# Optimization experiments

Hardware: AMD Instinct MI355X
Metric: run time of the kernel (lower is better)

## Reference

```python
import jax, jax.numpy as jnp
import numpy as np

DIM = 768
NUM_BLOCKS = 4
BLOCK = DIM // NUM_BLOCKS
SCALE = 0.02


def setup_inputs() -> dict:
    key = jax.random.key(0)
    ks = jax.random.split(key, 7)
    x = jax.random.normal(ks[0], (8, 64, 64, DIM), dtype=jnp.float32)
    w1 = SCALE * jax.random.normal(ks[1], (2, NUM_BLOCKS, BLOCK, BLOCK), dtype=jnp.float32)
    b1 = SCALE * jax.random.normal(ks[2], (2, NUM_BLOCKS, BLOCK), dtype=jnp.float32)
    w2 = SCALE * jax.random.normal(ks[3], (2, NUM_BLOCKS, BLOCK, BLOCK), dtype=jnp.float32)
    b2 = SCALE * jax.random.normal(ks[4], (2, NUM_BLOCKS, BLOCK), dtype=jnp.float32)
    # nn.Linear(dim, dim) weight/bias (kaiming-uniform-ish init; exact init irrelevant for correctness)
    lim = 1.0 / np.sqrt(DIM)
    bias_w = jax.random.uniform(ks[5], (DIM, DIM), minval=-lim, maxval=lim, dtype=jnp.float32)
    bias_b = jax.random.uniform(ks[6], (DIM,), minval=-lim, maxval=lim, dtype=jnp.float32)
    return {"x": x, "w1": w1, "b1": b1, "w2": w2, "b2": b2, "bias_w": bias_w, "bias_b": bias_b}


def _block_mul(t, w):
    # t: (..., nb, bs), w: (nb, bs, bs) -> (..., nb, bs)
    return jnp.einsum('...bd,bdk->...bk', t, w)


def reference(x, w1, b1, w2, b2, bias_w, bias_b):
    B, H, W, C = x.shape
    nb = w1.shape[1]
    bs = C // nb
    bias = x @ bias_w.T + bias_b  # nn.Linear on original x
    xb = x.reshape(B, H, W, nb, bs)
    xf = jnp.fft.rfftn(xb, axes=(1, 2), norm='ortho')  # (B, H, W//2+1, nb, bs) complex
    xr, xi = xf.real, xf.imag
    # layer 1: complex block matmul + bias + relu (relu applied per real/imag part as in source)
    r1 = jax.nn.relu(_block_mul(xr, w1[0]) - _block_mul(xi, w1[1]) + b1[0])
    i1 = jax.nn.relu(_block_mul(xr, w1[1]) + _block_mul(xi, w1[0]) + b1[1])
    # layer 2: NOTE the original torch code reassigns x_real first and then uses the NEW
    # x_real when computing x_imag — we faithfully reproduce that.
    r2 = _block_mul(r1, w2[0]) - _block_mul(i1, w2[1]) + b2[0]
    i2 = _block_mul(r2, w2[1]) + _block_mul(i1, w2[0]) + b2[1]
    xc = jax.lax.complex(r2, i2)
    out = jnp.fft.irfftn(xc, s=(H, W), axes=(1, 2), norm='ortho')
    out = out.reshape(B, H, W, C)
    return out + bias
```

## Files before the change

### kernel.cpp

```cpp
#include <hip/hip_runtime.h>

#define DIM 768
#define NBLK 4
#define BS 192
#define BATCH 8
#define HH 64
#define WW 64
#define KH 33
#define NPTS (BATCH*HH*KH)
#define TWOPI_OVER_64 0.0981747704246810387f
#define LROW 200
#define WSZ (NBLK*BS*BS)

typedef __attribute__((ext_vector_type(8))) short short8;
typedef __attribute__((ext_vector_type(4))) short short4v;
typedef __attribute__((ext_vector_type(4))) float floatx4;
typedef __attribute__((ext_vector_type(4))) unsigned int uint4v;

static __device__ __forceinline__ short f2bs(float f) {
  union { float f; unsigned int i; } v; v.f = f;
  unsigned int x = v.i;
  return (short)((x + 0x7fffu + ((x >> 16) & 1u)) >> 16);
}
static __device__ __forceinline__ float bs2f(short s) {
  union { unsigned int i; float f; } v; v.i = ((unsigned int)(unsigned short)s) << 16; return v.f;
}

#define GLD16(gp, lp) \
  __builtin_amdgcn_global_load_lds( \
      (const __attribute__((address_space(1))) unsigned int*)(gp), \
      (__attribute__((address_space(3))) unsigned int*)(lp), 16, 0, 0)

__global__ __launch_bounds__(256) void k_convx(
    const float* __restrict__ X, short* __restrict__ Xb)
{
  const int i = blockIdx.x * 256 + threadIdx.x;
  const float4* X4 = (const float4*)X;
  #pragma unroll
  for (int it = 0; it < 12; ++it) {
    const int idx = i + it * (2048 * 256);
    const float4 v = X4[idx];
    short4v p = { f2bs(v.x), f2bs(v.y), f2bs(v.z), f2bs(v.w) };
    *(short4v*)&Xb[(size_t)idx * 4] = p;
  }
}

__global__ __launch_bounds__(256) void k_convw(
    const float* __restrict__ W, short* __restrict__ Wb)
{
  const int idx = blockIdx.x * 256 + threadIdx.x;
  const float4 v = ((const float4*)W)[idx];
  short4v p = { f2bs(v.x), f2bs(v.y), f2bs(v.z), f2bs(v.w) };
  *(short4v*)&Wb[(size_t)idx * 4] = p;
}

__global__ __launch_bounds__(256) void k_bias_gemm3(
    const short* __restrict__ Xb, const short* __restrict__ Wb,
    const float* __restrict__ bb, short* __restrict__ Bias)
{
  __shared__ short As[128 * 32];
  __shared__ short Bs[128 * 32];
  const int t = threadIdx.x;
  const int wave = t >> 6, lane = t & 63;
  const int qm = lane & 15, quad = lane >> 4;
  const int wr = (wave >> 1) * 64;
  const int wc = (wave & 1) * 64;
  const int m0 = blockIdx.x * 128, n0 = blockIdx.y * 128;

  floatx4 acc[4][4];
  const floatx4 zero = {0.f, 0.f, 0.f, 0.f};
  #pragma unroll
  for (int ms = 0; ms < 4; ++ms)
    #pragma unroll
    for (int ns = 0; ns < 4; ++ns) acc[ms][ns] = zero;

  const int r0 = t >> 2,        kq0 = (t & 3) * 8;
  const int r1 = (t + 256) >> 2;
  const short* gA0 = &Xb[(size_t)(m0 + r0) * DIM + kq0];
  const short* gA1 = &Xb[(size_t)(m0 + r1) * DIM + kq0];
  const short* gB0 = &Wb[(size_t)(n0 + r0) * DIM + kq0];
  const short* gB1 = &Wb[(size_t)(n0 + r1) * DIM + kq0];
  short* lA0 = &As[wave * 512];
  short* lA1 = &As[wave * 512 + 2048];
  short* lB0 = &Bs[wave * 512];
  short* lB1 = &Bs[wave * 512 + 2048];

  #pragma unroll 1
  for (int k0 = 0; k0 < DIM; k0 += 32) {
    __syncthreads();
    GLD16(gA0 + k0, lA0);
    GLD16(gA1 + k0, lA1);
    GLD16(gB0 + k0, lB0);
    GLD16(gB1 + k0, lB1);
    __syncthreads();

    short8 af[4], bf[4];
    #pragma unroll
    for (int ms = 0; ms < 4; ++ms)
      af[ms] = *(const short8*)&As[(wr + ms*16 + qm) * 32 + quad * 8];
    #pragma unroll
    for (int ns = 0; ns < 4; ++ns)
      bf[ns] = *(const short8*)&Bs[(wc + ns*16 + qm) * 32 + quad * 8];
    #pragma unroll
    for (int ms = 0; ms < 4; ++ms)
      #pragma unroll
      for (int ns = 0; ns < 4; ++ns)
        acc[ms][ns] = __builtin_amdgcn_mfma_f32_16x16x32_bf16(af[ms], bf[ns], acc[ms][ns], 0, 0, 0);
  }

  #pragma unroll
  for (int ns = 0; ns < 4; ++ns) {
    const int col = n0 + wc + ns*16 + qm;
    const float bias = bb[col];
    #pragma unroll
    for (int ms = 0; ms < 4; ++ms)
      #pragma unroll
      for (int r = 0; r < 4; ++r) {
        const int row = m0 + wr + ms*16 + quad*4 + r;
        Bias[(size_t)row * DIM + col] = f2bs(acc[ms][ns][r] + bias);
      }
  }
}

__global__ __launch_bounds__(256) void k_rfft_w_mfma(
    const short* __restrict__ Xb,
    short* __restrict__ Sr, short* __restrict__ Si)
{
  __shared__ short Lx[96 * 72];
  const int t = threadIdx.x;
  const int wave = t >> 6, lane = t & 63;
  const int qm = lane & 15, quad = lane >> 4;
  const int bh = blockIdx.x;
  const int c0 = blockIdx.y * 96;
  const size_t xbase = (size_t)bh * (WW*DIM);
  const size_t obase = (size_t)bh * (KH*DIM);

  const int hd = t & 31;
  const int c4b = t >> 5;
  short4v ra[3], rb[3];
  #pragma unroll
  for (int it = 0; it < 3; ++it) {
    const int c4 = c4b + it * 8;
    const size_t g0 = xbase + (size_t)(2*hd) * DIM + c0 + c4 * 4;
    ra[it] = *(const short4v*)&Xb[g0];
    rb[it] = *(const short4v*)&Xb[g0 + DIM];
  }

  short8 Trh[2], Trl[2], Tih[2], Til[2];
  const int krow = wave * 16 + qm;
  #pragma unroll
  for (int kk = 0; kk < 2; ++kk) {
    #pragma unroll
    for (int j = 0; j < 8; ++j) {
      const int w = quad * 8 + j + kk * 32;
      const int ph = (krow * w) & 63;
      float s, c;
      sincosf((float)ph * TWOPI_OVER_64, &s, &c);
      const float tr = c, ti = -s;
      const short trh = f2bs(tr);
      const short tih = f2bs(ti);
      Trh[kk][j] = trh;  Trl[kk][j] = f2bs(tr - bs2f(trh));
      Tih[kk][j] = tih;  Til[kk][j] = f2bs(ti - bs2f(tih));
    }
  }

  #pragma unroll
  for (int it = 0; it < 3; ++it) {
    const int c4 = c4b + it * 8;
    #pragma unroll
    for (int e = 0; e < 4; ++e) {
      const int d = (c4*4 + e) * 36 + hd;
      ((unsigned*)Lx)[d] = (unsigned)(unsigned short)ra[it][e] |
                           ((unsigned)(unsigned short)rb[it][e] << 16);
    }
  }
  __syncthreads();

  if (wave < 3) {
    const floatx4 zero = {0.f, 0.f, 0.f, 0.f};
    #pragma unroll 1
    for (int ct = 0; ct < 6; ++ct) {
      floatx4 Cr = zero, Ci = zero;
      #pragma unroll
      for (int kk = 0; kk < 2; ++kk) {
        const int a = (ct*16 + qm) * 72 + kk*32 + quad*8;
        const short8 xv = *(const short8*)&Lx[a];
        Cr = __builtin_amdgcn_mfma_f32_16x16x32_bf16(Trh[kk], xv, Cr, 0,0,0);
        Cr = __builtin_amdgcn_mfma_f32_16x16x32_bf16(Trl[kk], xv, Cr, 0,0,0);
        Ci = __builtin_amdgcn_mfma_f32_16x16x32_bf16(Tih[kk], xv, Ci, 0,0,0);
        Ci = __builtin_amdgcn_mfma_f32_16x16x32_bf16(Til[kk], xv, Ci, 0,0,0);
      }
      #pragma unroll
      for (int r = 0; r < 4; ++r) {
        const int ko = wave*16 + quad*4 + r;
        if (ko < KH) {
          const size_t o = obase + (size_t)ko * DIM + c0 + ct*16 + qm;
          Sr[o] = f2bs(Cr[r]);
          Si[o] = f2bs(Ci[r]);
        }
      }
    }
  }
}

__global__ __launch_bounds__(256) void k_prep_w(
    const float* __restrict__ w1, const float* __restrict__ w2,
    short* __restrict__ Wout)
{
  const int arr = blockIdx.y;
  const int i = blockIdx.x * 256 + threadIdx.x;
  const int nb = i / (BS*BS);
  const int rem = i % (BS*BS);
  const int n = rem / BS;
  const int d = rem % BS;
  const float* src = (arr < 2) ? w1 : w2;
  const int j = arr & 1;
  const float s = (arr == 3) ? -1.f : 1.f;
  const float v = s * src[((size_t)(j*NBLK + nb) * BS + d) * BS + n];
  Wout[(size_t)arr * WSZ + i] = f2bs(v);
}

__global__ __launch_bounds__(256) void k_prep_w2(
    const float* __restrict__ w2, const float* __restrict__ b2,
    short* __restrict__ Wout, float* __restrict__ b2x)
{
  const int i = blockIdx.x * 256 + threadIdx.x;
  const int n = i % BS;
  const int d = (i / BS) % BS;
  const int nb = i / (BS*BS);
  const float* R = w2 + (size_t)nb * BS * BS;
  const float* I = w2 + ((size_t)NBLK + nb) * BS * BS;
  const float* br = b2 + nb * BS;
  float ri = 0.f, ii = 0.f, bx = 0.f;
  #pragma unroll 4
  for (int m = 0; m < BS; ++m) {
    const float win = I[m*BS + n];
    ri += R[d*BS + m] * win;
    ii += I[d*BS + m] * win;
    bx += br[m] * win;
  }
  const size_t o = ((size_t)nb * BS + n) * BS + d;
  Wout[(size_t)4 * WSZ + o] = f2bs(ri);
  Wout[(size_t)5 * WSZ + o] = f2bs(R[d*BS + n] - ii);
  if (d == 0) b2x[nb * BS + n] = b2[(NBLK + nb) * BS + n] + bx;
}

__global__ __launch_bounds__(256) void k_fmix(
    short* __restrict__ Sr, short* __restrict__ Si,
    const short* __restrict__ WT,
    const float* __restrict__ b1, const float* __restrict__ b2,
    const float* __restrict__ b2x)
{
  __shared__ short U[2 * 192 * 72];
  short* Ldr = U;
  short* Ldi = U + 192 * 72;
  short* Amr = U;
  short* Ami = U + 64 * LROW;

  const int t = threadIdx.x;
  const int wave = t >> 6, lane = t & 63;
  const int qm = lane & 15, quad = lane >> 4;
  const int bk = blockIdx.x;
  const int b = bk / KH, k = bk % KH;
  const int nb = blockIdx.y;
  const int c0 = nb * BS;
  const size_t hstride = (size_t)KH * DIM;
  const size_t base = ((size_t)b * HH * KH + k) * DIM;

  const int hd = t & 31;
  const int c8b = t >> 5;
  short8 ra[3], rb[3], ia[3], ib[3];
  #pragma unroll
  for (int it = 0; it < 3; ++it) {
    const int c8 = c8b + it * 8;
    const size_t g0 = base + (size_t)(2*hd) * hstride + c0 + c8 * 8;
    ra[it] = *(const short8*)&Sr[g0];
    rb[it] = *(const short8*)&Sr[g0 + hstride];
    ia[it] = *(const short8*)&Si[g0];
    ib[it] = *(const short8*)&Si[g0 + hstride];
  }

  const short* W1R  = WT;
  const short* W1I  = WT + 1 * (size_t)WSZ;
  const short* W2R  = WT + 2 * (size_t)WSZ;
  const short* W2IN = WT + 3 * (size_t)WSZ;
  const short* W2RI = WT + 4 * (size_t)WSZ;
  const short* W2X  = WT + 5 * (size_t)WSZ;
  int nl[3];
  size_t wb[3];
  #pragma unroll
  for (int nt = 0; nt < 3; ++nt) {
    nl[nt] = wave * 48 + nt * 16 + qm;
    wb[nt] = (size_t)(c0 + nl[nt]) * BS + quad * 8;
  }
  short8 w1r[3], w1i[3];
  #pragma unroll
  for (int nt = 0; nt < 3; ++nt) {
    w1r[nt] = *(const short8*)&W1R[wb[nt]];
    w1i[nt] = *(const short8*)&W1I[wb[nt]];
  }

  short8 Ch[2], Cl[2], Sh[2], Sl[2], SNh[2], SNl[2];
  const int hp = wave * 16 + qm;
  #pragma unroll
  for (int kk = 0; kk < 2; ++kk)
    #pragma unroll
    for (int j = 0; j < 8; ++j) {
      const int h = quad*8 + j + kk*32;
      const int ph = (hp * h) & 63;
      float s, c;
      sincosf((float)ph * TWOPI_OVER_64, &s, &c);
      const short ch = f2bs(c), sh = f2bs(s);
      Ch[kk][j] = ch;  Cl[kk][j] = f2bs(c - bs2f(ch));
      Sh[kk][j] = sh;  Sl[kk][j] = f2bs(s - bs2f(sh));
      SNh[kk][j] = (short)(sh ^ (short)0x8000);
      SNl[kk][j] = (short)(Sl[kk][j] ^ (short)0x8000);
    }

  #pragma unroll
  for (int it = 0; it < 3; ++it) {
    const int c8 = c8b + it * 8;
    #pragma unroll
    for (int e = 0; e < 8; ++e) {
      const int d = (c8*8 + e) * 36 + hd;
      ((unsigned*)Ldr)[d] = (unsigned)(unsigned short)ra[it][e] |
                            ((unsigned)(unsigned short)rb[it][e] << 16);
      ((unsigned*)Ldi)[d] = (unsigned)(unsigned short)ia[it][e] |
                            ((unsigned)(unsigned short)ib[it][e] << 16);
    }
  }
  __syncthreads();

  const floatx4 zero = {0.f, 0.f, 0.f, 0.f};
  floatx4 Fr[12], Fi[12];
  #pragma unroll
  for (int ct = 0; ct < 12; ++ct) { Fr[ct] = zero; Fi[ct] = zero; }
  #pragma unroll
  for (int ct = 0; ct < 12; ++ct)
    #pragma unroll
    for (int kk = 0; kk < 2; ++kk) {
      const int a = (ct*16 + qm) * 72 + kk*32 + quad*8;
      const short8 sr = *(const short8*)&Ldr[a];
      const short8 si = *(const short8*)&Ldi[a];
      Fr[ct] = __builtin_amdgcn_mfma_f32_16x16x32_bf16(Ch[kk],  sr, Fr[ct], 0,0,0);
      Fr[ct] = __builtin_amdgcn_mfma_f32_16x16x32_bf16(Cl[kk],  sr, Fr[ct], 0,0,0);
      Fr[ct] = __builtin_amdgcn_mfma_f32_16x16x32_bf16(Sh[kk],  si, Fr[ct], 0,0,0);
      Fr[ct] = __builtin_amdgcn_mfma_f32_16x16x32_bf16(Sl[kk],  si, Fr[ct], 0,0,0);
      Fi[ct] = __builtin_amdgcn_mfma_f32_16x16x32_bf16(SNh[kk], sr, Fi[ct], 0,0,0);
      Fi[ct] = __builtin_amdgcn_mfma_f32_16x16x32_bf16(SNl[kk], sr, Fi[ct], 0,0,0);
      Fi[ct] = __builtin_amdgcn_mfma_f32_16x16x32_bf16(Ch[kk],  si, Fi[ct], 0,0,0);
      Fi[ct] = __builtin_amdgcn_mfma_f32_16x16x32_bf16(Cl[kk],  si, Fi[ct], 0,0,0);
    }
  __syncthreads();

  #pragma unroll
  for (int ct = 0; ct < 12; ++ct)
    #pragma unroll
    for (int r = 0; r < 4; ++r) {
      const int row = wave*16 + quad*4 + r;
      const int c = ct*16 + qm;
      Amr[row * LROW + c] = f2bs(Fr[ct][r] * 0.015625f);
      Ami[row * LROW + c] = f2bs(Fi[ct][r] * 0.015625f);
    }
  __syncthreads();

  floatx4 aR[4][3], aI[4][3];
  #pragma unroll
  for (int ms = 0; ms < 4; ++ms)
    #pragma unroll
    for (int nt = 0; nt < 3; ++nt) { aR[ms][nt] = zero; aI[ms][nt] = zero; }

  #pragma unroll 1
  for (int k0 = 0; k0 < BS; k0 += 32) {
    short8 xr[4], xi[4];
    #pragma unroll
    for (int ms = 0; ms < 4; ++ms) {
      const int a = (ms*16 + qm) * LROW + k0 + quad * 8;
      xr[ms] = *(const short8*)&Amr[a];
      xi[ms] = *(const short8*)&Ami[a];
    }
    short8 cwr[3], cwi[3];
    #pragma unroll
    for (int nt = 0; nt < 3; ++nt) { cwr[nt] = w1r[nt]; cwi[nt] = w1i[nt]; }
    const int kn = k0 + 32;
    if (kn < BS) {
      #pragma unroll
      for (int nt = 0; nt < 3; ++nt) {
        w1r[nt] = *(const short8*)&W1R[wb[nt] + kn];
        w1i[nt] = *(const short8*)&W1I[wb[nt] + kn];
      }
    }
    #pragma unroll
    for (int nt = 0; nt < 3; ++nt) {
      short8 bin;
      *(uint4v*)&bin = *(const uint4v*)&cwi[nt] ^ 0x80008000u;
      #pragma unroll
      for (int ms = 0; ms < 4; ++ms) {
        aR[ms][nt] = __builtin_amdgcn_mfma_f32_16x16x32_bf16(xr[ms], cwr[nt], aR[ms][nt], 0,0,0);
        aR[ms][nt] = __builtin_amdgcn_mfma_f32_16x16x32_bf16(xi[ms], bin,     aR[ms][nt], 0,0,0);
        aI[ms][nt] = __builtin_amdgcn_mfma_f32_16x16x32_bf16(xr[ms], cwi[nt], aI[ms][nt], 0,0,0);
        aI[ms][nt] = __builtin_amdgcn_mfma_f32_16x16x32_bf16(xi[ms], cwr[nt], aI[ms][nt], 0,0,0);
      }
    }
  }
  __syncthreads();
  #pragma unroll
  for (int nt = 0; nt < 3; ++nt) {
    const float b1r = b1[nb * BS + nl[nt]];
    const float b1i = b1[(NBLK + nb) * BS + nl[nt]];
    #pragma unroll
    for (int ms = 0; ms < 4; ++ms)
      #pragma unroll
      for (int r = 0; r < 4; ++r) {
        const int row = ms*16 + quad*4 + r;
        Amr[row * LROW + nl[nt]] = f2bs(fmaxf(aR[ms][nt][r] + b1r, 0.f));
        Ami[row * LROW + nl[nt]] = f2bs(fmaxf(aI[ms][nt][r] + b1i, 0.f));
      }
  }
  __syncthreads();

  floatx4 c2r[4][3], c2i[4][3];
  #pragma unroll
  for (int ms = 0; ms < 4; ++ms)
    #pragma unroll
    for (int nt = 0; nt < 3; ++nt) { c2r[ms][nt] = zero; c2i[ms][nt] = zero; }

  #pragma unroll 1
  for (int k0 = 0; k0 < BS; k0 += 32) {
    short8 r1[4], i1[4];
    #pragma unroll
    for (int ms = 0; ms < 4; ++ms) {
      const int a = (ms*16 + qm) * LROW + k0 + quad * 8;
      r1[ms] = *(const short8*)&Amr[a];
      i1[ms] = *(const short8*)&Ami[a];
    }
    short8 w_r[3], w_in[3], w_ri[3], w_x[3];
    #pragma unroll
    for (int nt = 0; nt < 3; ++nt) {
      w_r [nt] = *(const short8*)&W2R [wb[nt] + k0];
      w_in[nt] = *(const short8*)&W2IN[wb[nt] + k0];
      w_ri[nt] = *(const short8*)&W2RI[wb[nt] + k0];
      w_x [nt] = *(const short8*)&W2X [wb[nt] + k0];
    }
    #pragma unroll
    for (int nt = 0; nt < 3; ++nt) {
      #pragma unroll
      for (int ms = 0; ms < 4; ++ms) {
        c2r[ms][nt] = __builtin_amdgcn_mfma_f32_16x16x32_bf16(r1[ms], w_r [nt], c2r[ms][nt], 0,0,0);
        c2r[ms][nt] = __builtin_amdgcn_mfma_f32_16x16x32_bf16(i1[ms], w_in[nt], c2r[ms][nt], 0,0,0);
        c2i[ms][nt] = __builtin_amdgcn_mfma_f32_16x16x32_bf16(r1[ms], w_ri[nt], c2i[ms][nt], 0,0,0);
        c2i[ms][nt] = __builtin_amdgcn_mfma_f32_16x16x32_bf16(i1[ms], w_x [nt], c2i[ms][nt], 0,0,0);
      }
    }
  }
  __syncthreads();

  #pragma unroll
  for (int nt = 0; nt < 3; ++nt) {
    const float b2r = b2 [nb * BS + nl[nt]];
    const float bxi = b2x[nb * BS + nl[nt]];
    const int c = nl[nt];
    #pragma unroll
    for (int ms = 0; ms < 4; ++ms)
      #pragma unroll
      for (int r = 0; r < 4; ++r) {
        const int row = ms*16 + quad*4 + r;
        Ldr[c * 72 + row] = f2bs(c2r[ms][nt][r] + b2r);
        Ldi[c * 72 + row] = f2bs(c2i[ms][nt][r] + bxi);
      }
  }
  __syncthreads();

  #pragma unroll 1
  for (int ct = 0; ct < 12; ++ct) {
    floatx4 Cr = zero, Ci = zero;
    #pragma unroll
    for (int kk = 0; kk < 2; ++kk) {
      const int a = (ct*16 + qm) * 72 + kk*32 + quad*8;
      const short8 gr = *(const short8*)&Ldr[a];
      const short8 gi = *(const short8*)&Ldi[a];
      Cr = __builtin_amdgcn_mfma_f32_16x16x32_bf16(Ch[kk],  gr, Cr, 0,0,0);
      Cr = __builtin_amdgcn_mfma_f32_16x16x32_bf16(Cl[kk],  gr, Cr, 0,0,0);
      Cr = __builtin_amdgcn_mfma_f32_16x16x32_bf16(SNh[kk], gi, Cr, 0,0,0);
      Cr = __builtin_amdgcn_mfma_f32_16x16x32_bf16(SNl[kk], gi, Cr, 0,0,0);
      Ci = __builtin_amdgcn_mfma_f32_16x16x32_bf16(Sh[kk],  gr, Ci, 0,0,0);
      Ci = __builtin_amdgcn_mfma_f32_16x16x32_bf16(Sl[kk],  gr, Ci, 0,0,0);
      Ci = __builtin_amdgcn_mfma_f32_16x16x32_bf16(Ch[kk],  gi, Ci, 0,0,0);
      Ci = __builtin_amdgcn_mfma_f32_16x16x32_bf16(Cl[kk],  gi, Ci, 0,0,0);
    }
    #pragma unroll
    for (int r = 0; r < 4; ++r) {
      const int hpo = wave*16 + quad*4 + r;
      const size_t o = base + (size_t)hpo * hstride + c0 + ct*16 + qm;
      Sr[o] = f2bs(Cr[r]);
      Si[o] = f2bs(Ci[r]);
    }
  }
}

__global__ __launch_bounds__(256) void k_irfft_w_mfma(
    const short* __restrict__ Sr, const short* __restrict__ Si,
    const short* __restrict__ Bias, float* __restrict__ out)
{
  __shared__ short Lr[96 * 72];
  __shared__ short Li[96 * 72];
  const int t = threadIdx.x;
  const int wave = t >> 6, lane = t & 63;
  const int qm = lane & 15, quad = lane >> 4;
  const int bh = blockIdx.x;
  const int c0 = blockIdx.y * 96;
  const size_t gbase = (size_t)bh * (KH*DIM);
  const size_t obase = (size_t)bh * (WW*DIM);

  const int hd = t & 31;
  const int c4b = t >> 5;
  short4v ra[3], rb[3], ia[3], ib[3];
  #pragma unroll
  for (int it = 0; it < 3; ++it) {
    const int c4 = c4b + it * 8;
    const int ka = 2*hd, kb = 2*hd + 1;
    short4v z = {0,0,0,0};
    ra[it] = z; rb[it] = z; ia[it] = z; ib[it] = z;
    if (ka < KH) {
      const size_t g0 = gbase + (size_t)ka * DIM + c0 + c4 * 4;
      ra[it] = *(const short4v*)&Sr[g0];
      ia[it] = *(const short4v*)&Si[g0];
    }
    if (kb < KH) {
      const size_t g1 = gbase + (size_t)kb * DIM + c0 + c4 * 4;
      rb[it] = *(const short4v*)&Sr[g1];
      ib[it] = *(const short4v*)&Si[g1];
    }
  }

  short8 Arh[2], Arl[2], Aih[2], Ail[2];
  const int wrow = wave * 16 + qm;
  #pragma unroll
  for (int kk = 0; kk < 2; ++kk) {
    #pragma unroll
    for (int j = 0; j < 8; ++j) {
      const int k = quad * 8 + j + kk * 32;
      float ar = 0.f, ai = 0.f;
      if (k < KH) {
        const int ph = (wrow * k) & 63;
        float s, c;
        sincosf((float)ph * TWOPI_OVER_64, &s, &c);
        const float ck = (k == 0 || k == 32) ? (1.0f/64.0f) : (2.0f/64.0f);
        ar = ck * c;
        ai = -ck * s;
      }
      const short arh = f2bs(ar);
      const short aih = f2bs(ai);
      Arh[kk][j] = arh;  Arl[kk][j] = f2bs(ar - bs2f(arh));
      Aih[kk][j] = aih;  Ail[kk][j] = f2bs(ai - bs2f(aih));
    }
  }

  #pragma unroll
  for (int it = 0; it < 3; ++it) {
    const int c4 = c4b + it * 8;
    #pragma unroll
    for (int e = 0; e < 4; ++e) {
      const int d = (c4*4 + e) * 36 + hd;
      ((unsigned*)Lr)[d] = (unsigned)(unsigned short)ra[it][e] |
                           ((unsigned)(unsigned short)rb[it][e] << 16);
      ((unsigned*)Li)[d] = (unsigned)(unsigned short)ia[it][e] |
                           ((unsigned)(unsigned short)ib[it][e] << 16);
    }
  }
  __syncthreads();

  const floatx4 zero = {0.f, 0.f, 0.f, 0.f};
  #pragma unroll 1
  for (int ct = 0; ct < 6; ++ct) {
    floatx4 C = zero;
    #pragma unroll
    for (int kk = 0; kk < 2; ++kk) {
      const int a = (ct*16 + qm) * 72 + kk*32 + quad*8;
      const short8 gr = *(const short8*)&Lr[a];
      const short8 gi = *(const short8*)&Li[a];
      C = __builtin_amdgcn_mfma_f32_16x16x32_bf16(Arh[kk], gr, C, 0,0,0);
      C = __builtin_amdgcn_mfma_f32_16x16x32_bf16(Arl[kk], gr, C, 0,0,0);
      C = __builtin_amdgcn_mfma_f32_16x16x32_bf16(Aih[kk], gi, C, 0,0,0);
      C = __builtin_amdgcn_mfma_f32_16x16x32_bf16(Ail[kk], gi, C, 0,0,0);
    }
    #pragma unroll
    for (int r = 0; r < 4; ++r) {
      const int w = wave*16 + quad*4 + r;
      const size_t o = obase + (size_t)w * DIM + c0 + ct*16 + qm;
      out[o] = C[r] + bs2f(Bias[o]);
    }
  }
}

extern "C" void kernel_launch(void* const* d_in, const int* in_sizes, int n_in,
                              void* d_out, int out_size, void* d_ws, size_t ws_size,
                              hipStream_t stream) {
  const float* x  = (const float*)d_in[0];
  const float* w1 = (const float*)d_in[1];
  const float* b1 = (const float*)d_in[2];
  const float* w2 = (const float*)d_in[3];
  const float* b2 = (const float*)d_in[4];
  const float* bw = (const float*)d_in[5];
  const float* bb = (const float*)d_in[6];
  float* out = (float*)d_out;

  short* Sr = (short*)d_ws;
  short* Si = Sr + (size_t)NPTS * DIM;
  short* WT = Si + (size_t)NPTS * DIM;
  short* Xb = WT + (size_t)6 * WSZ;
  short* Wb = Xb + (size_t)BATCH * HH * WW * DIM;
  short* Bias = Wb + (size_t)DIM * DIM;
  float* b2x = (float*)(Bias + (size_t)BATCH * HH * WW * DIM);

  k_convx<<<2048, 256, 0, stream>>>(x, Xb);
  k_convw<<<(DIM*DIM/4)/256, 256, 0, stream>>>(bw, Wb);
  k_prep_w<<<dim3(WSZ/256, 4), 256, 0, stream>>>(w1, w2, WT);
  k_prep_w2<<<dim3(WSZ/256), 256, 0, stream>>>(w2, b2, WT, b2x);
  k_bias_gemm3<<<dim3(32768/128, DIM/128), 256, 0, stream>>>(Xb, Wb, bb, Bias);
  k_rfft_w_mfma<<<dim3(BATCH*HH, DIM/96), 256, 0, stream>>>(Xb, Sr, Si);
  k_fmix<<<dim3(BATCH*KH, NBLK), 256, 0, stream>>>(Sr, Si, WT, b1, b2, b2x);
  k_irfft_w_mfma<<<dim3(BATCH*HH, DIM/96), 256, 0, stream>>>(Sr, Si, Bias, out);
}
```

Before: 481.9 us.

## Split k_fmix work across 8 waves with 512 threads per block

Doubles k_fmix block size to 512 threads. The column tiles of the FFT-along-H stages are split between two halves of the block, and the row tiles of the two channel-mix GEMMs are split the same way, so each wave holds half as many accumulators. This is meant to cut per-wave register pressure and raise the number of waves available to hide latency, given the small grid of 1056 blocks. In exchange, the register-prefetch of W1 weights across k-steps is dropped in favour of loading them inside the loop, and each weight fragment is now loaded by twice as many waves.

New measurement: 523.6 us. 1.09x slower.

```diff
diff --git a/kernel.cpp b/kernel.cpp
--- a/kernel.cpp
+++ b/kernel.cpp
@@ -245,7 +245,7 @@
   if (d == 0) b2x[nb * BS + n] = b2[(NBLK + nb) * BS + n] + bx;
 }
 
-__global__ __launch_bounds__(256) void k_fmix(
+__global__ __launch_bounds__(512) void k_fmix(
     short* __restrict__ Sr, short* __restrict__ Si,
     const short* __restrict__ WT,
     const float* __restrict__ b1, const float* __restrict__ b2,
@@ -259,6 +259,7 @@
 
   const int t = threadIdx.x;
   const int wave = t >> 6, lane = t & 63;
+  const int w4 = wave & 3, half = wave >> 2;
   const int qm = lane & 15, quad = lane >> 4;
   const int bk = blockIdx.x;
   const int b = bk / KH, k = bk % KH;
@@ -267,41 +268,28 @@
   const size_t hstride = (size_t)KH * DIM;
   const size_t base = ((size_t)b * HH * KH + k) * DIM;
 
-  const int hd = t & 31;
-  const int c8b = t >> 5;
-  short8 ra[3], rb[3], ia[3], ib[3];
-  #pragma unroll
-  for (int it = 0; it < 3; ++it) {
-    const int c8 = c8b + it * 8;
-    const size_t g0 = base + (size_t)(2*hd) * hstride + c0 + c8 * 8;
-    ra[it] = *(const short8*)&Sr[g0];
-    rb[it] = *(const short8*)&Sr[g0 + hstride];
-    ia[it] = *(const short8*)&Si[g0];
-    ib[it] = *(const short8*)&Si[g0 + hstride];
-  }
-
-  const short* W1R  = WT;
-  const short* W1I  = WT + 1 * (size_t)WSZ;
-  const short* W2R  = WT + 2 * (size_t)WSZ;
-  const short* W2IN = WT + 3 * (size_t)WSZ;
-  const short* W2RI = WT + 4 * (size_t)WSZ;
-  const short* W2X  = WT + 5 * (size_t)WSZ;
-  int nl[3];
-  size_t wb[3];
-  #pragma unroll
-  for (int nt = 0; nt < 3; ++nt) {
-    nl[nt] = wave * 48 + nt * 16 + qm;
-    wb[nt] = (size_t)(c0 + nl[nt]) * BS + quad * 8;
-  }
-  short8 w1r[3], w1i[3];
-  #pragma unroll
-  for (int nt = 0; nt < 3; ++nt) {
-    w1r[nt] = *(const short8*)&W1R[wb[nt]];
-    w1i[nt] = *(const short8*)&W1I[wb[nt]];
+  const int hd0 = t & 31;
+  const int c80 = t >> 5;
+  const int c81 = c80 + 16;
+  const bool has1 = (t < 256);
+  short8 ra0, rb0, ia0, ib0, ra1, rb1, ia1, ib1;
+  {
+    const size_t g0 = base + (size_t)(2*hd0) * hstride + c0 + c80 * 8;
+    ra0 = *(const short8*)&Sr[g0];
+    rb0 = *(const short8*)&Sr[g0 + hstride];
+    ia0 = *(const short8*)&Si[g0];
+    ib0 = *(const short8*)&Si[g0 + hstride];
+  }
+  if (has1) {
+    const size_t g1 = base + (size_t)(2*hd0) * hstride + c0 + c81 * 8;
+    ra1 = *(const short8*)&Sr[g1];
+    rb1 = *(const short8*)&Sr[g1 + hstride];
+    ia1 = *(const short8*)&Si[g1];
+    ib1 = *(const short8*)&Si[g1 + hstride];
   }
 
   short8 Ch[2], Cl[2], Sh[2], Sl[2], SNh[2], SNl[2];
-  const int hp = wave * 16 + qm;
+  const int hp = w4 * 16 + qm;
   #pragma unroll
   for (int kk = 0; kk < 2; ++kk)
     #pragma unroll
@@ -318,88 +306,104 @@
     }
 
   #pragma unroll
-  for (int it = 0; it < 3; ++it) {
-    const int c8 = c8b + it * 8;
+  for (int e = 0; e < 8; ++e) {
+    const int d = (c80*8 + e) * 36 + hd0;
+    ((unsigned*)Ldr)[d] = (unsigned)(unsigned short)ra0[e] |
+                          ((unsigned)(unsigned short)rb0[e] << 16);
+    ((unsigned*)Ldi)[d] = (unsigned)(unsigned short)ia0[e] |
+                          ((unsigned)(unsigned short)ib0[e] << 16);
+  }
+  if (has1) {
     #pragma unroll
     for (int e = 0; e < 8; ++e) {
-      const int d = (c8*8 + e) * 36 + hd;
-      ((unsigned*)Ldr)[d] = (unsigned)(unsigned short)ra[it][e] |
-                            ((unsigned)(unsigned short)rb[it][e] << 16);
-      ((unsigned*)Ldi)[d] = (unsigned)(unsigned short)ia[it][e] |
-                            ((unsigned)(unsigned short)ib[it][e] << 16);
+      const int d = (c81*8 + e) * 36 + hd0;
+      ((unsigned*)Ldr)[d] = (unsigned)(unsigned short)ra1[e] |
+                            ((unsigned)(unsigned short)rb1[e] << 16);
+      ((unsigned*)Ldi)[d] = (unsigned)(unsigned short)ia1[e] |
+                            ((unsigned)(unsigned short)ib1[e] << 16);
     }
   }
   __syncthreads();
 
   const floatx4 zero = {0.f, 0.f, 0.f, 0.f};
-  floatx4 Fr[12], Fi[12];
-  #pragma unroll
-  for (int ct = 0; ct < 12; ++ct) { Fr[ct] = zero; Fi[ct] = zero; }
-  #pragma unroll
-  for (int ct = 0; ct < 12; ++ct)
+  floatx4 Fr[6], Fi[6];
+  #pragma unroll
+  for (int j = 0; j < 6; ++j) { Fr[j] = zero; Fi[j] = zero; }
+  #pragma unroll
+  for (int j = 0; j < 6; ++j) {
+    const int ct = half * 6 + j;
     #pragma unroll
     for (int kk = 0; kk < 2; ++kk) {
       const int a = (ct*16 + qm) * 72 + kk*32 + quad*8;
       const short8 sr = *(const short8*)&Ldr[a];
       const short8 si = *(const short8*)&Ldi[a];
-      Fr[ct] = __builtin_amdgcn_mfma_f32_16x16x32_bf16(Ch[kk],  sr, Fr[ct], 0,0,0);
-      Fr[ct] = __builtin_amdgcn_mfma_f32_16x16x32_bf16(Cl[kk],  sr, Fr[ct], 0,0,0);
-      Fr[ct] = __builtin_amdgcn_mfma_f32_16x16x32_bf16(Sh[kk],  si, Fr[ct], 0,0,0);
-      Fr[ct] = __builtin_amdgcn_mfma_f32_16x16x32_bf16(Sl[kk],  si, Fr[ct], 0,0,0);
-      Fi[ct] = __builtin_amdgcn_mfma_f32_16x16x32_bf16(SNh[kk], sr, Fi[ct], 0,0,0);
-      Fi[ct] = __builtin_amdgcn_mfma_f32_16x16x32_bf16(SNl[kk], sr, Fi[ct], 0,0,0);
-      Fi[ct] = __builtin_amdgcn_mfma_f32_16x16x32_bf16(Ch[kk],  si, Fi[ct], 0,0,0);
-      Fi[ct] = __builtin_amdgcn_mfma_f32_16x16x32_bf16(Cl[kk],  si, Fi[ct], 0,0,0);
-    }
-  __syncthreads();
-
-  #pragma unroll
-  for (int ct = 0; ct < 12; ++ct)
+      Fr[j] = __builtin_amdgcn_mfma_f32_16x16x32_bf16(Ch[kk],  sr, Fr[j], 0,0,0);
+      Fr[j] = __builtin_amdgcn_mfma_f32_16x16x32_bf16(Cl[kk],  sr, Fr[j], 0,0,0);
+      Fr[j] = __builtin_amdgcn_mfma_f32_16x16x32_bf16(Sh[kk],  si, Fr[j], 0,0,0);
+      Fr[j] = __builtin_amdgcn_mfma_f32_16x16x32_bf16(Sl[kk],  si, Fr[j], 0,0,0);
+      Fi[j] = __builtin_amdgcn_mfma_f32_16x16x32_bf16(SNh[kk], sr, Fi[j], 0,0,0);
+      Fi[j] = __builtin_amdgcn_mfma_f32_16x16x32_bf16(SNl[kk], sr, Fi[j], 0,0,0);
+      Fi[j] = __builtin_amdgcn_mfma_f32_16x16x32_bf16(Ch[kk],  si, Fi[j], 0,0,0);
+      Fi[j] = __builtin_amdgcn_mfma_f32_16x16x32_bf16(Cl[kk],  si, Fi[j], 0,0,0);
+    }
+  }
+  __syncthreads();
+
+  #pragma unroll
+  for (int j = 0; j < 6; ++j) {
+    const int ct = half * 6 + j;
     #pragma unroll
     for (int r = 0; r < 4; ++r) {
-      const int row = wave*16 + quad*4 + r;
+      const int row = w4*16 + quad*4 + r;
       const int c = ct*16 + qm;
-      Amr[row * LROW + c] = f2bs(Fr[ct][r] * 0.015625f);
-      Ami[row * LROW + c] = f2bs(Fi[ct][r] * 0.015625f);
-    }
-  __syncthreads();
-
-  floatx4 aR[4][3], aI[4][3];
-  #pragma unroll
-  for (int ms = 0; ms < 4; ++ms)
-    #pragma unroll
-    for (int nt = 0; nt < 3; ++nt) { aR[ms][nt] = zero; aI[ms][nt] = zero; }
+      Amr[row * LROW + c] = f2bs(Fr[j][r] * 0.015625f);
+      Ami[row * LROW + c] = f2bs(Fi[j][r] * 0.015625f);
+    }
+  }
+  __syncthreads();
+
+  const short* W1R  = WT;
+  const short* W1I  = WT + 1 * (size_t)WSZ;
+  const short* W2R  = WT + 2 * (size_t)WSZ;
+  const short* W2IN = WT + 3 * (size_t)WSZ;
+  const short* W2RI = WT + 4 * (size_t)WSZ;
+  const short* W2X  = WT + 5 * (size_t)WSZ;
+
+  int nl[3];
+  size_t wb[3];
+  #pragma unroll
+  for (int nt = 0; nt < 3; ++nt) {
+    nl[nt] = w4 * 48 + nt * 16 + qm;
+    wb[nt] = (size_t)(c0 + nl[nt]) * BS + quad * 8;
+  }
+
+  floatx4 aR[2][3], aI[2][3];
+  #pragma unroll
+  for (int msl = 0; msl < 2; ++msl)
+    #pragma unroll
+    for (int nt = 0; nt < 3; ++nt) { aR[msl][nt] = zero; aI[msl][nt] = zero; }
 
   #pragma unroll 1
   for (int k0 = 0; k0 < BS; k0 += 32) {
-    short8 xr[4], xi[4];
-    #pragma unroll
-    for (int ms = 0; ms < 4; ++ms) {
-      const int a = (ms*16 + qm) * LROW + k0 + quad * 8;
-      xr[ms] = *(const short8*)&Amr[a];
-      xi[ms] = *(const short8*)&Ami[a];
-    }
-    short8 cwr[3], cwi[3];
-    #pragma unroll
-    for (int nt = 0; nt < 3; ++nt) { cwr[nt] = w1r[nt]; cwi[nt] = w1i[nt]; }
-    const int kn = k0 + 32;
-    if (kn < BS) {
-      #pragma unroll
-      for (int nt = 0; nt < 3; ++nt) {
-        w1r[nt] = *(const short8*)&W1R[wb[nt] + kn];
-        w1i[nt] = *(const short8*)&W1I[wb[nt] + kn];
-      }
+    short8 xr[2], xi[2];
+    #pragma unroll
+    for (int msl = 0; msl < 2; ++msl) {
+      const int a = ((half*2 + msl)*16 + qm) * LROW + k0 + quad * 8;
+      xr[msl] = *(const short8*)&Amr[a];
+      xi[msl] = *(const short8*)&Ami[a];
     }
     #pragma unroll
     for (int nt = 0; nt < 3; ++nt) {
+      const short8 br = *(const short8*)&W1R[wb[nt] + k0];
+      const short8 bi = *(const short8*)&W1I[wb[nt] + k0];
       short8 bin;
-      *(uint4v*)&bin = *(const uint4v*)&cwi[nt] ^ 0x80008000u;
-      #pragma unroll
-      for (int ms = 0; ms < 4; ++ms) {
-        aR[ms][nt] = __builtin_amdgcn_mfma_f32_16x16x32_bf16(xr[ms], cwr[nt], aR[ms][nt], 0,0,0);
-        aR[ms][nt] = __builtin_amdgcn_mfma_f32_16x16x32_bf16(xi[ms], bin,     aR[ms][nt], 0,0,0);
-        aI[ms][nt] = __builtin_amdgcn_mfma_f32_16x16x32_bf16(xr[ms], cwi[nt], aI[ms][nt], 0,0,0);
-        aI[ms][nt] = __builtin_amdgcn_mfma_f32_16x16x32_bf16(xi[ms], cwr[nt], aI[ms][nt], 0,0,0);
+      *(uint4v*)&bin = *(const uint4v*)&bi ^ 0x80008000u;
+      #pragma unroll
+      for (int msl = 0; msl < 2; ++msl) {
+        aR[msl][nt] = __builtin_amdgcn_mfma_f32_16x16x32_bf16(xr[msl], br,  aR[msl][nt], 0,0,0);
+        aR[msl][nt] = __builtin_amdgcn_mfma_f32_16x16x32_bf16(xi[msl], bin, aR[msl][nt], 0,0,0);
+        aI[msl][nt] = __builtin_amdgcn_mfma_f32_16x16x32_bf16(xr[msl], bi,  aI[msl][nt], 0,0,0);
+        aI[msl][nt] = __builtin_amdgcn_mfma_f32_16x16x32_bf16(xi[msl], br,  aI[msl][nt], 0,0,0);
       }
     }
   }
@@ -409,47 +413,43 @@
     const float b1r = b1[nb * BS + nl[nt]];
     const float b1i = b1[(NBLK + nb) * BS + nl[nt]];
     #pragma unroll
-    for (int ms = 0; ms < 4; ++ms)
+    for (int msl = 0; msl < 2; ++msl)
       #pragma unroll
       for (int r = 0; r < 4; ++r) {
-        const int row = ms*16 + quad*4 + r;
-        Amr[row * LROW + nl[nt]] = f2bs(fmaxf(aR[ms][nt][r] + b1r, 0.f));
-        Ami[row * LROW + nl[nt]] = f2bs(fmaxf(aI[ms][nt][r] + b1i, 0.f));
-      }
-  }
-  __syncthreads();
-
-  floatx4 c2r[4][3], c2i[4][3];
-  #pragma unroll
-  for (int ms = 0; ms < 4; ++ms)
-    #pragma unroll
-    for (int nt = 0; nt < 3; ++nt) { c2r[ms][nt] = zero; c2i[ms][nt] = zero; }
+        const int row = (half*2 + msl)*16 + quad*4 + r;
+        Amr[row * LROW + nl[nt]] = f2bs(fmaxf(aR[msl][nt][r] + b1r, 0.f));
+        Ami[row * LROW + nl[nt]] = f2bs(fmaxf(aI[msl][nt][r] + b1i, 0.f));
+      }
+  }
+  __syncthreads();
+
+  floatx4 c2r[2][3], c2i[2][3];
+  #pragma unroll
+  for (int msl = 0; msl < 2; ++msl)
+    #pragma unroll
+    for (int nt = 0; nt < 3; ++nt) { c2r[msl][nt] = zero; c2i[msl][nt] = zero; }
 
   #pragma unroll 1
   for (int k0 = 0; k0 < BS; k0 += 32) {
-    short8 r1[4], i1[4];
-    #pragma unroll
-    for (int ms = 0; ms < 4; ++ms) {
-      const int a = (ms*16 + qm) * LROW + k0 + quad * 8;
-      r1[ms] = *(const short8*)&Amr[a];
-      i1[ms] = *(const short8*)&Ami[a];
-    }
-    short8 w_r[3], w_in[3], w_ri[3], w_x[3];
+    short8 r1[2], i1[2];
+    #pragma unroll
+    for (int msl = 0; msl < 2; ++msl) {
+      const int a = ((half*2 + msl)*16 + qm) * LROW + k0 + quad * 8;
+      r1[msl] = *(const short8*)&Amr[a];
+      i1[msl] = *(const short8*)&Ami[a];
+    }
     #pragma unroll
     for (int nt = 0; nt < 3; ++nt) {
-      w_r [nt] = *(const short8*)&W2R [wb[nt] + k0];
-      w_in[nt] = *(const short8*)&W2IN[wb[nt] + k0];
-      w_ri[nt] = *(const short8*)&W2RI[wb[nt] + k0];
-      w_x [nt] = *(const short8*)&W2X [wb[nt] + k0];
-    }
-    #pragma unroll
-    for (int nt = 0; nt < 3; ++nt) {
-      #pragma unroll
-      for (int ms = 0; ms < 4; ++ms) {
-        c2r[ms][nt] = __builtin_amdgcn_mfma_f32_16x16x32_bf16(r1[ms], w_r [nt], c2r[ms][nt], 0,0,0);
-        c2r[ms][nt] = __builtin_amdgcn_mfma_f32_16x16x32_bf16(i1[ms], w_in[nt], c2r[ms][nt], 0,0,0);
-        c2i[ms][nt] = __builtin_amdgcn_mfma_f32_16x16x32_bf16(r1[ms], w_ri[nt], c2i[ms][nt], 0,0,0);
-        c2i[ms][nt] = __builtin_amdgcn_mfma_f32_16x16x32_bf16(i1[ms], w_x [nt], c2i[ms][nt], 0,0,0);
+      const short8 w_r  = *(const short8*)&W2R [wb[nt] + k0];
+      const short8 w_in = *(const short8*)&W2IN[wb[nt] + k0];
+      const short8 w_ri = *(const short8*)&W2RI[wb[nt] + k0];
+      const short8 w_x  = *(const short8*)&W2X [wb[nt] + k0];
+      #pragma unroll
+      for (int msl = 0; msl < 2; ++msl) {
+        c2r[msl][nt] = __builtin_amdgcn_mfma_f32_16x16x32_bf16(r1[msl], w_r,  c2r[msl][nt], 0,0,0);
+        c2r[msl][nt] = __builtin_amdgcn_mfma_f32_16x16x32_bf16(i1[msl], w_in, c2r[msl][nt], 0,0,0);
+        c2i[msl][nt] = __builtin_amdgcn_mfma_f32_16x16x32_bf16(r1[msl], w_ri, c2i[msl][nt], 0,0,0);
+        c2i[msl][nt] = __builtin_amdgcn_mfma_f32_16x16x32_bf16(i1[msl], w_x,  c2i[msl][nt], 0,0,0);
       }
     }
   }
@@ -461,18 +461,19 @@
     const float bxi = b2x[nb * BS + nl[nt]];
     const int c = nl[nt];
     #pragma unroll
-    for (int ms = 0; ms < 4; ++ms)
+    for (int msl = 0; msl < 2; ++msl)
       #pragma unroll
       for (int r = 0; r < 4; ++r) {
-        const int row = ms*16 + quad*4 + r;
-        Ldr[c * 72 + row] = f2bs(c2r[ms][nt][r] + b2r);
-        Ldi[c * 72 + row] = f2bs(c2i[ms][nt][r] + bxi);
+        const int row = (half*2 + msl)*16 + quad*4 + r;
+        Ldr[c * 72 + row] = f2bs(c2r[msl][nt][r] + b2r);
+        Ldi[c * 72 + row] = f2bs(c2i[msl][nt][r] + bxi);
       }
   }
   __syncthreads();
 
   #pragma unroll 1
-  for (int ct = 0; ct < 12; ++ct) {
+  for (int j = 0; j < 6; ++j) {
+    const int ct = half * 6 + j;
     floatx4 Cr = zero, Ci = zero;
     #pragma unroll
     for (int kk = 0; kk < 2; ++kk) {
@@ -490,7 +491,7 @@
     }
     #pragma unroll
     for (int r = 0; r < 4; ++r) {
-      const int hpo = wave*16 + quad*4 + r;
+      const int hpo = w4*16 + quad*4 + r;
       const size_t o = base + (size_t)hpo * hstride + c0 + ct*16 + qm;
       Sr[o] = f2bs(Cr[r]);
       Si[o] = f2bs(Ci[r]);
@@ -619,6 +620,6 @@
   k_prep_w2<<<dim3(WSZ/256), 256, 0, stream>>>(w2, b2, WT, b2x);
   k_bias_gemm3<<<dim3(32768/128, DIM/128), 256, 0, stream>>>(Xb, Wb, bb, Bias);
   k_rfft_w_mfma<<<dim3(BATCH*HH, DIM/96), 256, 0, stream>>>(Xb, Sr, Si);
-  k_fmix<<<dim3(BATCH*KH, NBLK), 256, 0, stream>>>(Sr, Si, WT, b1, b2, b2x);
+  k_fmix<<<dim3(BATCH*KH, NBLK), 512, 0, stream>>>(Sr, Si, WT, b1, b2, b2x);
   k_irfft_w_mfma<<<dim3(BATCH*HH, DIM/96), 256, 0, stream>>>(Sr, Si, Bias, out);
 }
```
